# Optimization experiments

Hardware: AMD Instinct MI355X
Metric: run time of the kernel (lower is better)

## Reference

```python
import jax, jax.numpy as jnp
import numpy as np

C, G, NH, NE = 640, 32, 8, 512
B, H, W, P = 8, 32, 32, 77
HD = C // NH
EPS = 1e-5


def _groupnorm(x, g, b):
    # x: (B, C, H, W); normalize over (C//G, H, W) within each of G groups
    bb, cc, hh, ww = x.shape
    xg = x.reshape(bb, G, cc // G, hh, ww)
    mu = xg.mean(axis=(2, 3, 4), keepdims=True)
    var = xg.var(axis=(2, 3, 4), keepdims=True)
    xg = (xg - mu) * jax.lax.rsqrt(var + EPS)
    return xg.reshape(bb, cc, hh, ww) * g[None, :, None, None] + b[None, :, None, None]


def _layernorm(x, g, b):
    mu = x.mean(axis=-1, keepdims=True)
    var = x.var(axis=-1, keepdims=True)
    return (x - mu) * jax.lax.rsqrt(var + EPS) * g + b


def _split_heads(t):
    # (B, S, C) -> (B, NH, S, HD)
    bb, ss, _ = t.shape
    return t.reshape(bb, ss, NH, HD).transpose(0, 2, 1, 3)


def _attn(q, k, v):
    # q,k,v: (B, NH, S, HD) — manual softmax(q k^T / sqrt(d)) v, as in the source
    scores = jnp.einsum('bhqd,bhkd->bhqk', q, k) / (HD ** 0.5)
    probs = jax.nn.softmax(scores, axis=-1)
    out = jnp.einsum('bhqk,bhkd->bhqd', probs, v)
    bb = q.shape[0]
    return out.transpose(0, 2, 1, 3).reshape(bb, q.shape[2], C)


def unet_attention_fwd(x, p, gn_g, gn_b, ci_w, ci_b, ln1_g, ln1_b,
                       qkv_w, qkv_b, saw_w, saw_b, ln2_g, ln2_b,
                       caq_w, caq_b, cak_w, cak_b, cav_w, cav_b, caw_w, caw_b,
                       ln3_g, ln3_b, g1_w, g1_b, g2_w, g2_b, co_w, co_b):
    residue_long = x
    h = _groupnorm(x, gn_g, gn_b)
    # conv_input: 1x1 conv == per-pixel linear; ci_w: (C_in, C_out)
    h = jnp.einsum('bihw,io->bohw', h, ci_w) + ci_b[None, :, None, None]
    bb, cc, hh, ww = h.shape
    h = h.reshape(bb, cc, hh * ww).transpose(0, 2, 1)  # (B, HW, C)

    # self attention
    res = h
    t = _layernorm(h, ln1_g, ln1_b)
    qkv = t @ qkv_w + qkv_b
    q, k, v = jnp.split(qkv, 3, axis=-1)
    t = _attn(_split_heads(q), _split_heads(k), _split_heads(v))
    h = res + (t @ saw_w + saw_b)

    # cross attention (prompt p: (B, 77, NE))
    res = h
    t = _layernorm(h, ln2_g, ln2_b)
    q = t @ caq_w + caq_b
    k = p @ cak_w + cak_b
    v = p @ cav_w + cav_b
    t = _attn(_split_heads(q), _split_heads(k), _split_heads(v))
    h = res + (t @ caw_w + caw_b)

    # GEGLU MLP (exact GELU, matching torch F.gelu default)
    res = h
    t = _layernorm(h, ln3_g, ln3_b)
    proj = t @ g1_w + g1_b  # (B, HW, 8C)
    a, gate = jnp.split(proj, 2, axis=-1)
    t = a * jax.nn.gelu(gate, approximate=False)
    h = res + (t @ g2_w + g2_b)

    h = h.transpose(0, 2, 1).reshape(bb, cc, hh, ww)
    out = jnp.einsum('bihw,io->bohw', h, co_w) + co_b[None, :, None, None]
    return out + residue_long


def setup_inputs() -> dict:
    keys = jax.random.split(jax.random.key(0), 20)
    ki = iter(keys)
    s = 0.02

    def w(shape):
        return jax.random.normal(next(ki), shape, jnp.float32) * s

    return {
        'x': jax.random.normal(next(ki), (B, C, H, W), jnp.float32),
        'p': jax.random.normal(next(ki), (B, P, NE), jnp.float32),
        'gn_g': jnp.ones((C,), jnp.float32), 'gn_b': jnp.zeros((C,), jnp.float32),
        'ci_w': w((C, C)), 'ci_b': jnp.zeros((C,), jnp.float32),
        'ln1_g': jnp.ones((C,), jnp.float32), 'ln1_b': jnp.zeros((C,), jnp.float32),
        'qkv_w': w((C, 3 * C)), 'qkv_b': jnp.zeros((3 * C,), jnp.float32),
        'saw_w': w((C, C)), 'saw_b': jnp.zeros((C,), jnp.float32),
        'ln2_g': jnp.ones((C,), jnp.float32), 'ln2_b': jnp.zeros((C,), jnp.float32),
        'caq_w': w((C, C)), 'caq_b': jnp.zeros((C,), jnp.float32),
        'cak_w': w((NE, C)), 'cak_b': jnp.zeros((C,), jnp.float32),
        'cav_w': w((NE, C)), 'cav_b': jnp.zeros((C,), jnp.float32),
        'caw_w': w((C, C)), 'caw_b': jnp.zeros((C,), jnp.float32),
        'ln3_g': jnp.ones((C,), jnp.float32), 'ln3_b': jnp.zeros((C,), jnp.float32),
        'g1_w': w((C, 8 * C)), 'g1_b': jnp.zeros((8 * C,), jnp.float32),
        'g2_w': w((4 * C, C)), 'g2_b': jnp.zeros((C,), jnp.float32),
        'co_w': w((C, C)), 'co_b': jnp.zeros((C,), jnp.float32),
    }


def reference(x, p, gn_g, gn_b, ci_w, ci_b, ln1_g, ln1_b,
              qkv_w, qkv_b, saw_w, saw_b, ln2_g, ln2_b,
              caq_w, caq_b, cak_w, cak_b, cav_w, cav_b, caw_w, caw_b,
              ln3_g, ln3_b, g1_w, g1_b, g2_w, g2_b, co_w, co_b):
    return unet_attention_fwd(x, p, gn_g, gn_b, ci_w, ci_b, ln1_g, ln1_b,
                              qkv_w, qkv_b, saw_w, saw_b, ln2_g, ln2_b,
                              caq_w, caq_b, cak_w, cak_b, cav_w, cav_b, caw_w, caw_b,
                              ln3_g, ln3_b, g1_w, g1_b, g2_w, g2_b, co_w, co_b)
```

## Files before the change

### kernel.cpp

```cpp
#include <hip/hip_runtime.h>
#include <math.h>

typedef unsigned short u16;
typedef __attribute__((ext_vector_type(8))) short short8;
typedef __attribute__((ext_vector_type(4))) float f32x4;

#define DI static __device__ __forceinline__

DI float bf2f(u16 u) { union { unsigned u; float f; } c; c.u = (unsigned)u << 16; return c.f; }
DI u16 f2bf(float f) {
  union { float f; unsigned u; } c; c.f = f;
  unsigned r = c.u + 0x7fffu + ((c.u >> 16) & 1u);
  return (u16)(r >> 16);
}

DI void gload16(const u16* g, u16* l) {
  __builtin_amdgcn_global_load_lds(
      (const __attribute__((address_space(1))) unsigned int*)g,
      (__attribute__((address_space(3))) unsigned int*)l, 16, 0, 0);
}

struct PrepDesc { const float* src; u16* dst; int K, N, nbx, boff, perm; };
struct PrepArgs { PrepDesc d[10]; };

__global__ __launch_bounds__(256) void prep_all(PrepArgs a) {
  int bid = blockIdx.x;
  int i = 0;
  while (i < 9 && bid >= a.d[i + 1].boff) i++;
  const PrepDesc D = a.d[i];
  int rel = bid - D.boff;
  int bx = rel % D.nbx, by = rel / D.nbx;
  int K = D.K, N = D.N;
  __shared__ float tile[32][33];
  int k0 = by * 32, n0 = bx * 32;
  int tid = threadIdx.x;
  int ni = tid & 31, ki8 = tid >> 5;
  for (int q = 0; q < 4; q++) {
    int k = ki8 + q * 8;
    tile[k][ni] = D.src[(size_t)(k0 + k) * N + n0 + ni];
  }
  __syncthreads();
  int kj = tid & 31, nj8 = tid >> 5;
  for (int q = 0; q < 4; q++) {
    int n = nj8 + q * 8;
    int nold = n0 + n;
    int rowp = nold;
    if (D.perm) {
      rowp = (nold < 2560) ? ((nold >> 5) * 64 + (nold & 31))
                           : (((nold - 2560) >> 5) * 64 + 32 + (nold & 31));
    }
    D.dst[(size_t)rowp * K + k0 + kj] = f2bf(tile[kj][n]);
  }
}

__global__ __launch_bounds__(256) void conv_bf16(const float* __restrict__ in,
                                                 u16* __restrict__ out, long n) {
  long i = (long)blockIdx.x * 256 + threadIdx.x;
  if (i < n) out[i] = f2bf(in[i]);
}

__global__ __launch_bounds__(256) void gn_stats(const float* __restrict__ x,
                                                float* __restrict__ mean_o,
                                                float* __restrict__ rstd_o) {
  int bg = blockIdx.x;
  const float4* p = (const float4*)(x + (size_t)bg * 20480);
  float s = 0.f, sq = 0.f;
  for (int i = threadIdx.x; i < 5120; i += 256) {
    float4 v = p[i];
    s += v.x + v.y + v.z + v.w;
    sq += v.x * v.x + v.y * v.y + v.z * v.z + v.w * v.w;
  }
  for (int off = 1; off < 64; off <<= 1) { s += __shfl_xor(s, off); sq += __shfl_xor(sq, off); }
  __shared__ float ps[4], pq[4];
  int w = threadIdx.x >> 6;
  if ((threadIdx.x & 63) == 0) { ps[w] = s; pq[w] = sq; }
  __syncthreads();
  if (threadIdx.x == 0) {
    float S = ps[0] + ps[1] + ps[2] + ps[3];
    float Q = pq[0] + pq[1] + pq[2] + pq[3];
    float mu = S / 20480.f;
    float var = Q / 20480.f - mu * mu;
    mean_o[bg] = mu;
    rstd_o[bg] = rsqrtf(var + 1e-5f);
  }
}

__global__ __launch_bounds__(256) void gn_apply(const float* __restrict__ x,
                                                const float* __restrict__ mean_,
                                                const float* __restrict__ rstd_,
                                                const float* __restrict__ g,
                                                const float* __restrict__ bb,
                                                u16* __restrict__ out) {
  __shared__ float tile[32][33];
  int b = blockIdx.z, c0 = blockIdx.y * 32, s0 = blockIdx.x * 32;
  int tid = threadIdx.x;
  int si = tid & 31, ci8 = tid >> 5;
  for (int i = 0; i < 4; i++) {
    int c = c0 + ci8 + i * 8;
    int gg = c / 20;
    float mu = mean_[b * 32 + gg], rs = rstd_[b * 32 + gg];
    float v = x[((size_t)b * 640 + c) * 1024 + s0 + si];
    tile[ci8 + i * 8][si] = (v - mu) * rs * g[c] + bb[c];
  }
  __syncthreads();
  int cj = tid & 31, sj8 = tid >> 5;
  for (int i = 0; i < 4; i++) {
    int sj = sj8 + i * 8;
    out[((size_t)b * 1024 + s0 + sj) * 640 + c0 + cj] = f2bf(tile[cj][sj]);
  }
}

__global__ __launch_bounds__(256) void ln_kernel(const float* __restrict__ in,
                                                 const float* __restrict__ g,
                                                 const float* __restrict__ bb,
                                                 u16* __restrict__ out) {
  int t = blockIdx.x * 4 + (threadIdx.x >> 6);
  int lane = threadIdx.x & 63;
  const float* row = in + (size_t)t * 640;
  float xv[10], s = 0.f, sq = 0.f;
  for (int j = 0; j < 10; j++) {
    xv[j] = row[lane + j * 64];
    s += xv[j];
    sq += xv[j] * xv[j];
  }
  for (int off = 1; off < 64; off <<= 1) { s += __shfl_xor(s, off); sq += __shfl_xor(sq, off); }
  float mu = s * (1.f / 640.f);
  float var = sq * (1.f / 640.f) - mu * mu;
  float rstd = rsqrtf(var + 1e-5f);
  for (int j = 0; j < 10; j++) {
    int c = lane + j * 64;
    out[(size_t)t * 640 + c] = f2bf((xv[j] - mu) * rstd * g[c] + bb[c]);
  }
}


DI const short8* fragp(const u16* unit, int row, int g4) {
  int off = row * 64 + g4 * 16;
  off ^= ((off >> 7) & 3) << 4;
  return (const short8*)((const char*)unit + off);
}

template <int MODE>
__global__ __launch_bounds__(512, 1) void gemm256(const u16* __restrict__ A,
                                                  const u16* __restrict__ Bt,
                                                  const float* __restrict__ bias,
                                                  void* outp, const float* res,
                                                  int M, int N, int K) {
  __shared__ __align__(16) u16 As[4][8192];
  __shared__ __align__(16) u16 Bs[4][8192];
  const int tid = threadIdx.x;
  const int lane = tid & 63, wid = tid >> 6;
  const int wm = wid >> 2, wn = wid & 3;
  const int rq = lane & 15, g4 = lane >> 4;
  const int m0 = blockIdx.x * 256, n0 = blockIdx.y * 256;

  int D0 = tid * 16;
  int so = D0 ^ (((D0 >> 7) & 3) << 4);
  const int srow = so >> 6;
  const int sk16 = (so & 63) >> 1;

  f32x4 acc[8][4] = {};
  const int nt = K >> 5;

#define STG_A(kt)                                                              \
  {                                                                            \
    gload16(A + (size_t)(m0 + srow) * K + (kt)*32 + sk16,                      \
            &As[(kt) & 3][0] + tid * 8);                                       \
    gload16(A + (size_t)(m0 + 128 + srow) * K + (kt)*32 + sk16,                \
            &As[(kt) & 3][4096] + tid * 8);                                    \
  }
#define STG_B(kt)                                                              \
  {                                                                            \
    gload16(Bt + (size_t)(n0 + srow) * K + (kt)*32 + sk16,                     \
            &Bs[(kt) & 3][0] + tid * 8);                                       \
    gload16(Bt + (size_t)(n0 + 128 + srow) * K + (kt)*32 + sk16,               \
            &Bs[(kt) & 3][4096] + tid * 8);                                    \
  }
#define BAR asm volatile("s_barrier" ::: "memory")

#define PH1(T, DO_STG)                                                         \
  {                                                                            \
    const u16* Au = &As[(T) & 3][0];                                           \
    const u16* Bu = &Bs[(T) & 3][0];                                           \
    _Pragma("unroll") for (int i = 0; i < 4; i++)                              \
        af[i] = *fragp(Au, wm * 128 + i * 16 + rq, g4);                        \
    _Pragma("unroll") for (int j = 0; j < 4; j++)                              \
        bf[j] = *fragp(Bu, wn * 64 + j * 16 + rq, g4);                         \
    if (DO_STG) STG_A((T) + 3);                                                \
    BAR;                                                                       \
    asm volatile("s_waitcnt lgkmcnt(0)" ::: "memory");                         \
    __builtin_amdgcn_s_setprio(1);                                             \
    _Pragma("unroll") for (int i = 0; i < 4; i++)                              \
        _Pragma("unroll") for (int j = 0; j < 4; j++)                          \
            acc[i][j] =                                                        \
        __builtin_amdgcn_mfma_f32_16x16x32_bf16(af[i], bf[j], acc[i][j], 0, 0, 0); \
    __builtin_amdgcn_s_setprio(0);                                             \
    BAR;                                                                       \
  }

#define PH2(T, DO_STG, WSTR)                                                   \
  {                                                                            \
    const u16* Au = &As[(T) & 3][0];                                           \
    _Pragma("unroll") for (int i = 0; i < 4; i++)                              \
        af[i] = *fragp(Au, wm * 128 + 64 + i * 16 + rq, g4);                   \
    if (DO_STG) STG_B((T) + 3);                                                \
    asm volatile(WSTR ::: "memory");                                           \
    BAR;                                                                       \
    asm volatile("s_waitcnt lgkmcnt(0)" ::: "memory");                         \
    __builtin_amdgcn_s_setprio(1);                                             \
    _Pragma("unroll") for (int i = 0; i < 4; i++)                              \
        _Pragma("unroll") for (int j = 0; j < 4; j++)                          \
            acc[4 + i][j] =                                                    \
        __builtin_amdgcn_mfma_f32_16x16x32_bf16(af[i], bf[j], acc[4 + i][j], 0, 0, 0); \
    __builtin_amdgcn_s_setprio(0);                                             \
    BAR;                                                                       \
  }

  STG_A(0); STG_B(0); STG_A(1); STG_B(1); STG_A(2); STG_B(2);
  asm volatile("s_waitcnt vmcnt(8)" ::: "memory");
  BAR;

  short8 af[4], bf[4];
  int t = 0;
  for (; t < nt - 3; t++) {
    PH1(t, true);
    PH2(t, true, "s_waitcnt vmcnt(8)");
  }
  PH1(t, false); PH2(t, false, "s_waitcnt vmcnt(4)"); t++;
  PH1(t, false); PH2(t, false, "s_waitcnt vmcnt(0)"); t++;
  PH1(t, false); PH2(t, false, "s_nop 0");

  if (MODE == 5) {
#pragma unroll
    for (int mf = 0; mf < 8; mf++) {
      int mb = m0 + wm * 128 + mf * 16 + g4 * 4;
#pragma unroll
      for (int j = 0; j < 2; j++) {
        int n = n0 + wn * 64 + j * 16 + rq;
        int c = (n >> 6) * 32 + (n & 31);
        float ba = bias[c];
        float bg = bias[2560 + c];
#pragma unroll
        for (int r = 0; r < 4; r++) {
          float a = acc[mf][j][r] + ba;
          float gt = acc[mf][j + 2][r] + bg;
          float gl = 0.5f * gt * (1.f + erff(gt * 0.70710678f));
          ((u16*)outp)[(size_t)(mb + r) * 2560 + c] = f2bf(a * gl);
        }
      }
    }
  } else {
#pragma unroll
    for (int mf = 0; mf < 8; mf++) {
#pragma unroll
      for (int j = 0; j < 4; j++) {
        int n = n0 + wn * 64 + j * 16 + rq;
        if (n >= N) continue;
        float bv = bias[n];
        int mb = m0 + wm * 128 + mf * 16 + g4 * 4;
        f32x4 v = acc[mf][j];
#pragma unroll
        for (int r = 0; r < 4; r++) {
          size_t o = (size_t)(mb + r) * N + n;
          ((u16*)outp)[o] = f2bf(v[r] + bv);
        }
      }
    }
  }
  (void)res;
#undef STG_A
#undef STG_B
#undef PH1
#undef PH2
#undef BAR
}

template <int MODE>
__global__ __launch_bounds__(256) void gemm_bt(const u16* __restrict__ A,
                                               const u16* __restrict__ Bt,
                                               const float* __restrict__ bias,
                                               void* outp, const float* res,
                                               int M, int N, int K) {
  __shared__ __align__(16) u16 As[2][128 * 32];
  __shared__ __align__(16) u16 Bs[2][128 * 32];
  const int tid = threadIdx.x;
  const int lane = tid & 63, wid = tid >> 6;
  const int wm = wid >> 1, wn = wid & 1;
  const int m0 = blockIdx.x * 128, n0 = blockIdx.y * 128;
  const int rq = lane & 15, g4 = lane >> 4;

  const int srow = tid >> 2;
  const int scol = tid & 3;
  int gmA0 = m0 + srow;        if (gmA0 >= M) gmA0 = M - 1;
  int gmA1 = m0 + 64 + srow;   if (gmA1 >= M) gmA1 = M - 1;
  const u16* gA0 = A + (size_t)gmA0 * K + scol * 8;
  const u16* gA1 = A + (size_t)gmA1 * K + scol * 8;
  const u16* gB0 = Bt + (size_t)(n0 + srow) * K + scol * 8;
  const u16* gB1 = Bt + (size_t)(n0 + 64 + srow) * K + scol * 8;
  u16* lA0 = &As[0][srow * 32 + scol * 8];
  u16* lA1 = &As[0][(64 + srow) * 32 + scol * 8];
  u16* lB0 = &Bs[0][srow * 32 + scol * 8];
  u16* lB1 = &Bs[0][(64 + srow) * 32 + scol * 8];

  f32x4 acc[4][4] = {};

  auto STAGE = [&](int buf, int k0) {
    int o = buf * (128 * 32);
    gload16(gA0 + k0, lA0 + o);
    gload16(gA1 + k0, lA1 + o);
    gload16(gB0 + k0, lB0 + o);
    gload16(gB1 + k0, lB1 + o);
  };
  auto COMPUTE = [&](int buf) {
    short8 af[4], bfr[4];
    for (int i = 0; i < 4; i++)
      af[i] = *(const short8*)&As[buf][(wm * 64 + i * 16 + rq) * 32 + g4 * 8];
    for (int j = 0; j < 4; j++)
      bfr[j] = *(const short8*)&Bs[buf][(wn * 64 + j * 16 + rq) * 32 + g4 * 8];
    __builtin_amdgcn_s_setprio(1);
    for (int i = 0; i < 4; i++)
      for (int j = 0; j < 4; j++)
        acc[i][j] = __builtin_amdgcn_mfma_f32_16x16x32_bf16(af[i], bfr[j], acc[i][j], 0, 0, 0);
    __builtin_amdgcn_s_setprio(0);
  };

  const int nk = K >> 5;
  STAGE(0, 0);
  int cur = 0;
  for (int t = 0; t < nk - 1; t++) {
    STAGE(cur ^ 1, (t + 1) << 5);
    asm volatile("s_waitcnt vmcnt(4)" ::: "memory");
    __builtin_amdgcn_s_barrier();
    COMPUTE(cur);
    __builtin_amdgcn_s_barrier();
    cur ^= 1;
  }
  asm volatile("s_waitcnt vmcnt(0)" ::: "memory");
  __builtin_amdgcn_s_barrier();
  COMPUTE(cur);

  for (int j = 0; j < 4; j++) {
    int n = n0 + wn * 64 + j * 16 + rq;
    float bv = bias[n];
    for (int i = 0; i < 4; i++) {
      int mb = m0 + wm * 64 + i * 16 + g4 * 4;
      f32x4 v = acc[i][j];
      if (MODE == 3) {
        int b = mb >> 10, sp = mb & 1023;
        size_t o = ((size_t)b * 640 + n) * 1024 + sp;
        f32x4 xv = *(const f32x4*)(res + o);
        f32x4 ov;
        for (int r = 0; r < 4; r++) ov[r] = v[r] + bv + xv[r];
        *(f32x4*)((float*)outp + o) = ov;
      } else {
        for (int r = 0; r < 4; r++) {
          int m = mb + r;
          if (m >= M) break;
          size_t o = (size_t)m * N + n;
          float val = v[r] + bv;
          if (MODE == 0)
            ((float*)outp)[o] = val;
          else if (MODE == 1)
            ((u16*)outp)[o] = f2bf(val);
          else if (MODE == 2)
            ((float*)outp)[o] = val + res[o];
          else
            ((u16*)outp)[o] = f2bf(val + res[o]);
        }
      }
    }
  }
}

__global__ __launch_bounds__(256) void attn_kernel(const u16* __restrict__ Qb, int ldq, long qbs,
                                                   const u16* __restrict__ Kb, int ldk, long kbs,
                                                   const u16* __restrict__ Vb,
                                                   u16* __restrict__ Ob, int ldo, long obs,
                                                   int Sk, float scale) {
  __shared__ __align__(16) u16 Ks[64 * 96];
  __shared__ __align__(16) u16 Vt[80 * 64];
  __shared__ __align__(16) u16 Ps[4][16 * 72];
  const short8 zero = {0, 0, 0, 0, 0, 0, 0, 0};
  const int tid = threadIdx.x;
  const int lane = tid & 63, w = tid >> 6;
  const int rq = lane & 15, g4 = lane >> 4;
  const int b = blockIdx.z, h = blockIdx.y;
  const u16* Q = Qb + (size_t)b * qbs + h * 80;
  const u16* Kp = Kb + (size_t)b * kbs + h * 80;
  const u16* Vp = Vb + (size_t)b * kbs + h * 80;
  u16* Op = Ob + (size_t)b * obs + h * 80;
  const int q0 = blockIdx.x * 64 + w * 16;
  const float Af = scale * 1.44269504f;

  short8 qa[3];
#pragma unroll
  for (int kk = 0; kk < 3; kk++) {
    int d = kk * 32 + g4 * 8;
    qa[kk] = (d < 80) ? *(const short8*)(Q + (size_t)(q0 + rq) * ldq + d) : zero;
  }
  f32x4 oacc[5] = {};
  float m_run = -1e30f, l_run = 0.f;

  const int nkt = (Sk + 63) >> 6;
  for (int kt = 0; kt < nkt; kt++) {
    const int kbase = kt * 64;
    for (int s = tid; s < 768; s += 256) {
      int row = s / 12, c = s % 12;
      int kidx = kbase + row;
      short8 v = zero;
      if (c < 10 && kidx < Sk) v = *(const short8*)(Kp + (size_t)kidx * ldk + c * 8);
      int byte = row * 192 + c * 16;
      byte ^= (row & 7) << 4;
      *(short8*)((char*)Ks + byte) = v;
    }
    for (int s = tid; s < 320; s += 256) {
      int k2 = (s & 31) * 2, c = s >> 5;
      int k0i = kbase + k2;
      short8 v0 = zero, v1 = zero;
      if (k0i < Sk) v0 = *(const short8*)(Vp + (size_t)k0i * ldk + c * 8);
      if (k0i + 1 < Sk) v1 = *(const short8*)(Vp + (size_t)(k0i + 1) * ldk + c * 8);
#pragma unroll
      for (int jj = 0; jj < 8; jj++) {
        int d = c * 8 + jj;
        unsigned cm = (unsigned)(u16)v0[jj] | ((unsigned)(u16)v1[jj] << 16);
        int byte = d * 128 + k2 * 2;
        byte ^= (d & 7) << 4;
        *(unsigned*)((char*)Vt + byte) = cm;
      }
    }
    __syncthreads();

    f32x4 sc[4] = {};
#pragma unroll
    for (int n = 0; n < 4; n++)
#pragma unroll
      for (int kk = 0; kk < 3; kk++) {
        int row = n * 16 + rq;
        int byte = row * 192 + (kk * 32 + g4 * 8) * 2;
        byte ^= (rq & 7) << 4;
        short8 kb = *(const short8*)((const char*)Ks + byte);
        sc[n] = __builtin_amdgcn_mfma_f32_16x16x32_bf16(kb, qa[kk], sc[n], 0, 0, 0);
      }
    const bool full = (kbase + 64 <= Sk);
    if (!full) {
#pragma unroll
      for (int n = 0; n < 4; n++)
#pragma unroll
        for (int r = 0; r < 4; r++)
          if (kbase + n * 16 + g4 * 4 + r >= Sk) sc[n][r] = -1e30f;
    }
    float t0 = fmaxf(fmaxf(sc[0][0], sc[0][1]), fmaxf(sc[0][2], sc[0][3]));
    float t1 = fmaxf(fmaxf(sc[1][0], sc[1][1]), fmaxf(sc[1][2], sc[1][3]));
    float t2 = fmaxf(fmaxf(sc[2][0], sc[2][1]), fmaxf(sc[2][2], sc[2][3]));
    float t3 = fmaxf(fmaxf(sc[3][0], sc[3][1]), fmaxf(sc[3][2], sc[3][3]));
    float tm = fmaxf(fmaxf(t0, t1), fmaxf(t2, t3));
    tm = fmaxf(tm, __shfl_xor(tm, 16));
    tm = fmaxf(tm, __shfl_xor(tm, 32));
    if (!__all(tm <= m_run + 48.0f)) {
      float mn = fmaxf(m_run, tm);
      float sf = exp2f(Af * (m_run - mn));
      m_run = mn;
      l_run *= sf;
      float sfo[4];
#pragma unroll
      for (int r = 0; r < 4; r++) sfo[r] = __shfl(sf, g4 * 4 + r);
#pragma unroll
      for (int nn = 0; nn < 5; nn++)
#pragma unroll
        for (int r = 0; r < 4; r++) oacc[nn][r] *= sfo[r];
    }
    const float Am = Af * m_run;
    float rs0 = 0.f, rs1 = 0.f;
#pragma unroll
    for (int n = 0; n < 4; n++) {
      float p0 = exp2f(fmaf(Af, sc[n][0], -Am));
      float p1 = exp2f(fmaf(Af, sc[n][1], -Am));
      float p2 = exp2f(fmaf(Af, sc[n][2], -Am));
      float p3 = exp2f(fmaf(Af, sc[n][3], -Am));
      sc[n][0] = p0; sc[n][1] = p1; sc[n][2] = p2; sc[n][3] = p3;
      rs0 += p0 + p1;
      rs1 += p2 + p3;
    }
    float rsum = rs0 + rs1;
    rsum += __shfl_xor(rsum, 16);
    rsum += __shfl_xor(rsum, 32);
    l_run += rsum;
#pragma unroll
    for (int n = 0; n < 4; n++) {
      unsigned pk0, pk1;
      asm("v_cvt_pk_bf16_f32 %0, %1, %2" : "=v"(pk0) : "v"(sc[n][0]), "v"(sc[n][1]));
      asm("v_cvt_pk_bf16_f32 %0, %1, %2" : "=v"(pk1) : "v"(sc[n][2]), "v"(sc[n][3]));
      int base = rq * 72 + n * 16 + g4 * 4;
      *(unsigned*)&Ps[w][base] = pk0;
      *(unsigned*)&Ps[w][base + 2] = pk1;
    }
    __builtin_amdgcn_s_setprio(1);
#pragma unroll
    for (int s = 0; s < 2; s++) {
      short8 pa = *(const short8*)&Ps[w][rq * 72 + s * 32 + g4 * 8];
#pragma unroll
      for (int nn = 0; nn < 5; nn++) {
        int row = nn * 16 + rq;
        int byte = row * 128 + (s * 32 + g4 * 8) * 2;
        byte ^= (rq & 7) << 4;
        short8 vb = *(const short8*)((const char*)Vt + byte);
        oacc[nn] = __builtin_amdgcn_mfma_f32_16x16x32_bf16(pa, vb, oacc[nn], 0, 0, 0);
      }
    }
    __builtin_amdgcn_s_setprio(0);
    __syncthreads();
  }
  float lo[4];
#pragma unroll
  for (int r = 0; r < 4; r++) lo[r] = 1.0f / __shfl(l_run, g4 * 4 + r);
#pragma unroll
  for (int nn = 0; nn < 5; nn++)
#pragma unroll
    for (int r = 0; r < 4; r++)
      Op[(size_t)(q0 + g4 * 4 + r) * ldo + nn * 16 + rq] = f2bf(oacc[nn][r] * lo[r]);
}

extern "C" void kernel_launch(void* const* d_in, const int* in_sizes, int n_in,
                              void* d_out, int out_size, void* d_ws, size_t ws_size,
                              hipStream_t stream) {
  (void)in_sizes; (void)n_in; (void)out_size; (void)ws_size;
  const float* x = (const float*)d_in[0];
  const float* p = (const float*)d_in[1];
  const float* gn_g = (const float*)d_in[2];
  const float* gn_b = (const float*)d_in[3];
  const float* ci_w = (const float*)d_in[4];
  const float* ci_b = (const float*)d_in[5];
  const float* ln1_g = (const float*)d_in[6];
  const float* ln1_b = (const float*)d_in[7];
  const float* qkv_w = (const float*)d_in[8];
  const float* qkv_b = (const float*)d_in[9];
  const float* saw_w = (const float*)d_in[10];
  const float* saw_b = (const float*)d_in[11];
  const float* ln2_g = (const float*)d_in[12];
  const float* ln2_b = (const float*)d_in[13];
  const float* caq_w = (const float*)d_in[14];
  const float* caq_b = (const float*)d_in[15];
  const float* cak_w = (const float*)d_in[16];
  const float* cak_b = (const float*)d_in[17];
  const float* cav_w = (const float*)d_in[18];
  const float* cav_b = (const float*)d_in[19];
  const float* caw_w = (const float*)d_in[20];
  const float* caw_b = (const float*)d_in[21];
  const float* ln3_g = (const float*)d_in[22];
  const float* ln3_b = (const float*)d_in[23];
  const float* g1_w = (const float*)d_in[24];
  const float* g1_b = (const float*)d_in[25];
  const float* g2_w = (const float*)d_in[26];
  const float* g2_b = (const float*)d_in[27];
  const float* co_w = (const float*)d_in[28];
  const float* co_b = (const float*)d_in[29];
  float* out = (float*)d_out;

  char* ws = (char*)d_ws;
  size_t off = 0;
  auto alloc = [&](size_t bytes) {
    size_t o = off;
    off += (bytes + 255) & ~(size_t)255;
    return o;
  };
  u16* WCI = (u16*)(ws + alloc((size_t)768 * 640 * 2));
  u16* WQKV = (u16*)(ws + alloc((size_t)2048 * 640 * 2));
  u16* WSAW = (u16*)(ws + alloc((size_t)768 * 640 * 2));
  u16* WCAQ = (u16*)(ws + alloc((size_t)768 * 640 * 2));
  u16* WCAK = (u16*)(ws + alloc((size_t)640 * 512 * 2));
  u16* WCAV = (u16*)(ws + alloc((size_t)640 * 512 * 2));
  u16* WCAW = (u16*)(ws + alloc((size_t)768 * 640 * 2));
  u16* WG1 = (u16*)(ws + alloc((size_t)5120 * 640 * 2));
  u16* WG2 = (u16*)(ws + alloc((size_t)768 * 2560 * 2));
  u16* WCO = (u16*)(ws + alloc((size_t)768 * 640 * 2));
  u16* X = (u16*)(ws + alloc((size_t)8192 * 640 * 2));
  u16* Y = (u16*)(ws + alloc((size_t)8192 * 640 * 2));
  float* F1 = (float*)(ws + alloc((size_t)8192 * 640 * 4));
  u16* QKV = (u16*)(ws + alloc((size_t)8192 * 1920 * 2));
  u16* PBF = (u16*)(ws + alloc((size_t)616 * 512 * 2));
  u16* KC = (u16*)(ws + alloc((size_t)616 * 640 * 2));
  u16* VC = (u16*)(ws + alloc((size_t)616 * 640 * 2));
  u16* TG = (u16*)(ws + alloc((size_t)8192 * 2560 * 2));
  float* GNM = (float*)(ws + alloc(256 * 4));
  float* GNR = (float*)(ws + alloc(256 * 4));

  PrepArgs pa;
  int boff = 0;
  auto addw = [&](int idx, const float* src, u16* dst, int K, int N, int perm) {
    pa.d[idx].src = src; pa.d[idx].dst = dst;
    pa.d[idx].K = K; pa.d[idx].N = N;
    pa.d[idx].nbx = N / 32; pa.d[idx].boff = boff; pa.d[idx].perm = perm;
    boff += (N / 32) * (K / 32);
  };
  addw(0, ci_w, WCI, 640, 640, 0);
  addw(1, qkv_w, WQKV, 640, 1920, 0);
  addw(2, saw_w, WSAW, 640, 640, 0);
  addw(3, caq_w, WCAQ, 640, 640, 0);
  addw(4, cak_w, WCAK, 512, 640, 0);
  addw(5, cav_w, WCAV, 512, 640, 0);
  addw(6, caw_w, WCAW, 640, 640, 0);
  addw(7, g1_w, WG1, 640, 5120, 1);
  addw(8, g2_w, WG2, 2560, 640, 0);
  addw(9, co_w, WCO, 640, 640, 0);
  prep_all<<<boff, 256, 0, stream>>>(pa);
  conv_bf16<<<1232, 256, 0, stream>>>(p, PBF, (long)616 * 512);

  gn_stats<<<256, 256, 0, stream>>>(x, GNM, GNR);
  gn_apply<<<dim3(32, 20, 8), 256, 0, stream>>>(x, GNM, GNR, gn_g, gn_b, X);

  const float scale = 0.11180339887498949f;

  gemm_bt<0><<<dim3(64, 5), 256, 0, stream>>>(X, WCI, ci_b, F1, nullptr, 8192, 640, 640);
  ln_kernel<<<2048, 256, 0, stream>>>(F1, ln1_g, ln1_b, Y);
  gemm256<1><<<dim3(32, 8), 512, 0, stream>>>(Y, WQKV, qkv_b, QKV, nullptr, 8192, 1920, 640);
  attn_kernel<<<dim3(16, 8, 8), 256, 0, stream>>>(QKV, 1920, (long)1024 * 1920,
                                                  QKV + 640, 1920, (long)1024 * 1920,
                                                  QKV + 1280, X, 640, (long)1024 * 640,
                                                  1024, scale);
  gemm_bt<2><<<dim3(64, 5), 256, 0, stream>>>(X, WSAW, saw_b, F1, F1, 8192, 640, 640);
  ln_kernel<<<2048, 256, 0, stream>>>(F1, ln2_g, ln2_b, Y);
  gemm_bt<1><<<dim3(64, 5), 256, 0, stream>>>(Y, WCAQ, caq_b, X, nullptr, 8192, 640, 640);
  gemm_bt<1><<<dim3(5, 5), 256, 0, stream>>>(PBF, WCAK, cak_b, KC, nullptr, 616, 640, 512);
  gemm_bt<1><<<dim3(5, 5), 256, 0, stream>>>(PBF, WCAV, cav_b, VC, nullptr, 616, 640, 512);
  attn_kernel<<<dim3(16, 8, 8), 256, 0, stream>>>(X, 640, (long)1024 * 640,
                                                  KC, 640, (long)77 * 640,
                                                  VC, Y, 640, (long)1024 * 640,
                                                  77, scale);
  gemm_bt<2><<<dim3(64, 5), 256, 0, stream>>>(Y, WCAW, caw_b, F1, F1, 8192, 640, 640);
  ln_kernel<<<2048, 256, 0, stream>>>(F1, ln3_g, ln3_b, X);
  gemm256<5><<<dim3(32, 20), 512, 0, stream>>>(X, WG1, g1_b, TG, nullptr, 8192, 5120, 640);
  gemm_bt<4><<<dim3(64, 5), 256, 0, stream>>>(TG, WG2, g2_b, X, F1, 8192, 640, 2560);
  gemm_bt<3><<<dim3(64, 5), 256, 0, stream>>>(X, WCO, co_b, out, x, 8192, 640, 640);
}
```

Baseline: 489.8 us.

## Add XCD block swizzle, deepen GEMM pipelines, fuse cross-attn K/V projections

Adds an XCD-aware block index remap to both GEMM kernels so neighbouring tiles land on the same chiplet and share L2. The 256-tile GEMM drops one barrier per phase and moves all prefetch into the second phase, with scheduling barriers added. The 128-tile GEMM moves from double to quad buffered LDS with a 2-ahead prefetch and one barrier per k-step. The cross-attention K and V projections are merged into a single GEMM with concatenated weights and bias. The deeper buffers raise LDS use, and fewer barriers risk buffer-reuse races if the prefetch distance is wrong.

```diff
diff --git a/kernel.cpp b/kernel.cpp
--- a/kernel.cpp
+++ b/kernel.cpp
@@ -18,6 +18,16 @@
   __builtin_amdgcn_global_load_lds(
       (const __attribute__((address_space(1))) unsigned int*)g,
       (__attribute__((address_space(3))) unsigned int*)l, 16, 0, 0);
+}
+
+DI void xcd_swz(int& bx, int& by, int gx, int gy) {
+  int id = by * gx + bx;
+  int n = gx * gy;
+  int q = n >> 3, r = n & 7;
+  int xcd = id & 7, k = id >> 3;
+  int s = (xcd < r) ? (xcd * (q + 1) + k) : (r * (q + 1) + (xcd - r) * q + k);
+  bx = s % gx;
+  by = s / gx;
 }
 
 struct PrepDesc { const float* src; u16* dst; int K, N, nbx, boff, perm; };
@@ -57,6 +67,14 @@
                                                  u16* __restrict__ out, long n) {
   long i = (long)blockIdx.x * 256 + threadIdx.x;
   if (i < n) out[i] = f2bf(in[i]);
+}
+
+__global__ __launch_bounds__(256) void concat2(const float* __restrict__ a,
+                                               const float* __restrict__ b,
+                                               float* __restrict__ o, int n) {
+  int i = blockIdx.x * 256 + threadIdx.x;
+  if (i < n) o[i] = a[i];
+  else if (i < 2 * n) o[i] = b[i - n];
 }
 
 __global__ __launch_bounds__(256) void gn_stats(const float* __restrict__ x,
@@ -152,7 +170,9 @@
   const int lane = tid & 63, wid = tid >> 6;
   const int wm = wid >> 2, wn = wid & 3;
   const int rq = lane & 15, g4 = lane >> 4;
-  const int m0 = blockIdx.x * 256, n0 = blockIdx.y * 256;
+  int bx = blockIdx.x, by = blockIdx.y;
+  xcd_swz(bx, by, gridDim.x, gridDim.y);
+  const int m0 = bx * 256, n0 = by * 256;
 
   int D0 = tid * 16;
   int so = D0 ^ (((D0 >> 7) & 3) << 4);
@@ -178,7 +198,7 @@
   }
 #define BAR asm volatile("s_barrier" ::: "memory")
 
-#define PH1(T, DO_STG)                                                         \
+#define PH1(T)                                                                 \
   {                                                                            \
     const u16* Au = &As[(T) & 3][0];                                           \
     const u16* Bu = &Bs[(T) & 3][0];                                           \
@@ -186,16 +206,15 @@
         af[i] = *fragp(Au, wm * 128 + i * 16 + rq, g4);                        \
     _Pragma("unroll") for (int j = 0; j < 4; j++)                              \
         bf[j] = *fragp(Bu, wn * 64 + j * 16 + rq, g4);                         \
-    if (DO_STG) STG_A((T) + 3);                                                \
     BAR;                                                                       \
     asm volatile("s_waitcnt lgkmcnt(0)" ::: "memory");                         \
+    __builtin_amdgcn_sched_barrier(0);                                         \
     __builtin_amdgcn_s_setprio(1);                                             \
     _Pragma("unroll") for (int i = 0; i < 4; i++)                              \
         _Pragma("unroll") for (int j = 0; j < 4; j++)                          \
             acc[i][j] =                                                        \
         __builtin_amdgcn_mfma_f32_16x16x32_bf16(af[i], bf[j], acc[i][j], 0, 0, 0); \
     __builtin_amdgcn_s_setprio(0);                                             \
-    BAR;                                                                       \
   }
 
 #define PH2(T, DO_STG, WSTR)                                                   \
@@ -203,17 +222,17 @@
     const u16* Au = &As[(T) & 3][0];                                           \
     _Pragma("unroll") for (int i = 0; i < 4; i++)                              \
         af[i] = *fragp(Au, wm * 128 + 64 + i * 16 + rq, g4);                   \
-    if (DO_STG) STG_B((T) + 3);                                                \
+    if (DO_STG) { STG_A((T) + 3); STG_B((T) + 3); }                            \
     asm volatile(WSTR ::: "memory");                                           \
     BAR;                                                                       \
     asm volatile("s_waitcnt lgkmcnt(0)" ::: "memory");                         \
+    __builtin_amdgcn_sched_barrier(0);                                         \
     __builtin_amdgcn_s_setprio(1);                                             \
     _Pragma("unroll") for (int i = 0; i < 4; i++)                              \
         _Pragma("unroll") for (int j = 0; j < 4; j++)                          \
             acc[4 + i][j] =                                                    \
         __builtin_amdgcn_mfma_f32_16x16x32_bf16(af[i], bf[j], acc[4 + i][j], 0, 0, 0); \
     __builtin_amdgcn_s_setprio(0);                                             \
-    BAR;                                                                       \
   }
 
   STG_A(0); STG_B(0); STG_A(1); STG_B(1); STG_A(2); STG_B(2);
@@ -223,12 +242,12 @@
   short8 af[4], bf[4];
   int t = 0;
   for (; t < nt - 3; t++) {
-    PH1(t, true);
+    PH1(t);
     PH2(t, true, "s_waitcnt vmcnt(8)");
   }
-  PH1(t, false); PH2(t, false, "s_waitcnt vmcnt(4)"); t++;
-  PH1(t, false); PH2(t, false, "s_waitcnt vmcnt(0)"); t++;
-  PH1(t, false); PH2(t, false, "s_nop 0");
+  PH1(t); PH2(t, false, "s_waitcnt vmcnt(4)"); t++;
+  PH1(t); PH2(t, false, "s_waitcnt vmcnt(0)"); t++;
+  PH1(t); PH2(t, false, "s_nop 0");
 
   if (MODE == 5) {
 #pragma unroll
@@ -281,12 +300,14 @@
                                                const float* __restrict__ bias,
                                                void* outp, const float* res,
                                                int M, int N, int K) {
-  __shared__ __align__(16) u16 As[2][128 * 32];
-  __shared__ __align__(16) u16 Bs[2][128 * 32];
+  __shared__ __align__(16) u16 As[4][128 * 32];
+  __shared__ __align__(16) u16 Bs[4][128 * 32];
   const int tid = threadIdx.x;
   const int lane = tid & 63, wid = tid >> 6;
   const int wm = wid >> 1, wn = wid & 1;
-  const int m0 = blockIdx.x * 128, n0 = blockIdx.y * 128;
+  int bx = blockIdx.x, by = blockIdx.y;
+  xcd_swz(bx, by, gridDim.x, gridDim.y);
+  const int m0 = bx * 128, n0 = by * 128;
   const int rq = lane & 15, g4 = lane >> 4;
 
   const int srow = tid >> 2;
@@ -326,18 +347,21 @@
 
   const int nk = K >> 5;
   STAGE(0, 0);
-  int cur = 0;
-  for (int t = 0; t < nk - 1; t++) {
-    STAGE(cur ^ 1, (t + 1) << 5);
-    asm volatile("s_waitcnt vmcnt(4)" ::: "memory");
+  STAGE(1, 32);
+  int t = 0;
+  for (; t < nk - 2; t++) {
+    STAGE((t + 2) & 3, (t + 2) << 5);
+    asm volatile("s_waitcnt vmcnt(8)" ::: "memory");
     __builtin_amdgcn_s_barrier();
-    COMPUTE(cur);
-    __builtin_amdgcn_s_barrier();
-    cur ^= 1;
-  }
+    COMPUTE(t & 3);
+  }
+  asm volatile("s_waitcnt vmcnt(4)" ::: "memory");
+  __builtin_amdgcn_s_barrier();
+  COMPUTE(t & 3);
+  t++;
   asm volatile("s_waitcnt vmcnt(0)" ::: "memory");
   __builtin_amdgcn_s_barrier();
-  COMPUTE(cur);
+  COMPUTE(t & 3);
 
   for (int j = 0; j < 4; j++) {
     int n = n0 + wn * 64 + j * 16 + rq;
@@ -567,8 +591,7 @@
   u16* WQKV = (u16*)(ws + alloc((size_t)2048 * 640 * 2));
   u16* WSAW = (u16*)(ws + alloc((size_t)768 * 640 * 2));
   u16* WCAQ = (u16*)(ws + alloc((size_t)768 * 640 * 2));
-  u16* WCAK = (u16*)(ws + alloc((size_t)640 * 512 * 2));
-  u16* WCAV = (u16*)(ws + alloc((size_t)640 * 512 * 2));
+  u16* WCAKV = (u16*)(ws + alloc((size_t)1280 * 512 * 2));
   u16* WCAW = (u16*)(ws + alloc((size_t)768 * 640 * 2));
   u16* WG1 = (u16*)(ws + alloc((size_t)5120 * 640 * 2));
   u16* WG2 = (u16*)(ws + alloc((size_t)768 * 2560 * 2));
@@ -578,11 +601,11 @@
   float* F1 = (float*)(ws + alloc((size_t)8192 * 640 * 4));
   u16* QKV = (u16*)(ws + alloc((size_t)8192 * 1920 * 2));
   u16* PBF = (u16*)(ws + alloc((size_t)616 * 512 * 2));
-  u16* KC = (u16*)(ws + alloc((size_t)616 * 640 * 2));
-  u16* VC = (u16*)(ws + alloc((size_t)616 * 640 * 2));
+  u16* KVC = (u16*)(ws + alloc((size_t)616 * 1280 * 2));
   u16* TG = (u16*)(ws + alloc((size_t)8192 * 2560 * 2));
   float* GNM = (float*)(ws + alloc(256 * 4));
   float* GNR = (float*)(ws + alloc(256 * 4));
+  float* CBIAS = (float*)(ws + alloc(1280 * 4));
 
   PrepArgs pa;
   int boff = 0;
@@ -596,14 +619,15 @@
   addw(1, qkv_w, WQKV, 640, 1920, 0);
   addw(2, saw_w, WSAW, 640, 640, 0);
   addw(3, caq_w, WCAQ, 640, 640, 0);
-  addw(4, cak_w, WCAK, 512, 640, 0);
-  addw(5, cav_w, WCAV, 512, 640, 0);
+  addw(4, cak_w, WCAKV, 512, 640, 0);
+  addw(5, cav_w, WCAKV + (size_t)640 * 512, 512, 640, 0);
   addw(6, caw_w, WCAW, 640, 640, 0);
   addw(7, g1_w, WG1, 640, 5120, 1);
   addw(8, g2_w, WG2, 2560, 640, 0);
   addw(9, co_w, WCO, 640, 640, 0);
   prep_all<<<boff, 256, 0, stream>>>(pa);
   conv_bf16<<<1232, 256, 0, stream>>>(p, PBF, (long)616 * 512);
+  concat2<<<5, 256, 0, stream>>>(cak_b, cav_b, CBIAS, 640);
 
   gn_stats<<<256, 256, 0, stream>>>(x, GNM, GNR);
   gn_apply<<<dim3(32, 20, 8), 256, 0, stream>>>(x, GNM, GNR, gn_g, gn_b, X);
@@ -620,11 +644,10 @@
   gemm_bt<2><<<dim3(64, 5), 256, 0, stream>>>(X, WSAW, saw_b, F1, F1, 8192, 640, 640);
   ln_kernel<<<2048, 256, 0, stream>>>(F1, ln2_g, ln2_b, Y);
   gemm_bt<1><<<dim3(64, 5), 256, 0, stream>>>(Y, WCAQ, caq_b, X, nullptr, 8192, 640, 640);
-  gemm_bt<1><<<dim3(5, 5), 256, 0, stream>>>(PBF, WCAK, cak_b, KC, nullptr, 616, 640, 512);
-  gemm_bt<1><<<dim3(5, 5), 256, 0, stream>>>(PBF, WCAV, cav_b, VC, nullptr, 616, 640, 512);
+  gemm_bt<1><<<dim3(5, 10), 256, 0, stream>>>(PBF, WCAKV, CBIAS, KVC, nullptr, 616, 1280, 512);
   attn_kernel<<<dim3(16, 8, 8), 256, 0, stream>>>(X, 640, (long)1024 * 640,
-                                                  KC, 640, (long)77 * 640,
-                                                  VC, Y, 640, (long)1024 * 640,
+                                                  KVC, 1280, (long)77 * 1280,
+                                                  KVC + 640, Y, 640, (long)1024 * 640,
                                                   77, scale);
   gemm_bt<2><<<dim3(64, 5), 256, 0, stream>>>(Y, WCAW, caw_b, F1, F1, 8192, 640, 640);
   ln_kernel<<<2048, 256, 0, stream>>>(F1, ln3_g, ln3_b, X);
```

Measured after the change: 475.2 us. 1.03x faster.
